# Performance work log

Measured on AMD Instinct MI355X. Metric: run time of the kernel, lower is better.

The kernel has to match this reference:

```python
import jax, jax.numpy as jnp
import numpy as np

B, L, D = 4, 4096, 256


def setup_inputs() -> dict:
    key = jax.random.key(0)
    kx, kq, kk, kv, ko = jax.random.split(key, 5)
    std = 0.02
    return {
        "x": jax.random.normal(kx, (B, L, D), dtype=jnp.float32),
        "Wq": std * jax.random.normal(kq, (D, D), dtype=jnp.float32),
        "Wk": std * jax.random.normal(kk, (D, D), dtype=jnp.float32),
        "Wv": std * jax.random.normal(kv, (D, D), dtype=jnp.float32),
        "Wo": std * jax.random.normal(ko, (D, D), dtype=jnp.float32),
    }


def reference(x, Wq, Wk, Wv, Wo):
    # nn.Linear(d,d,bias=False): y = x @ W.T
    q = x @ Wq.T  # [B,L,D]
    k = x @ Wk.T
    v = x @ Wv.T
    logits = jnp.einsum("bld,bmd->blm", q, k)  # [B,L,L], no 1/sqrt(d) scaling
    Lq = x.shape[1]
    causal_mask = jnp.triu(jnp.ones((Lq, Lq), dtype=bool), k=1)  # True above diag
    # ReLU attention: mask future to 0, relu, divide row i by max(i, 1)
    logits = jnp.where(causal_mask[None], jnp.asarray(0.0, logits.dtype), logits)
    attn = jax.nn.relu(logits)
    row_counts = jnp.maximum(jnp.arange(Lq, dtype=attn.dtype), 1.0)  # clamp_min(1)
    attn = attn / row_counts[None, :, None]
    ctx = jnp.einsum("blm,bmd->bld", attn, v)
    return ctx @ Wo.T
```

## Files before the change

kernel.cpp:

```cpp
#include <hip/hip_runtime.h>

#define BB 4
#define LL 4096
#define DD 256
#define MAXOFF 160

typedef short bf16x8 __attribute__((ext_vector_type(8)));
typedef short bf16x4 __attribute__((ext_vector_type(4)));
typedef float f32x4 __attribute__((ext_vector_type(4)));
typedef unsigned u32x4 __attribute__((ext_vector_type(4)));
typedef unsigned short u16;

__device__ inline u16 f2b(float f) {
    union { float f; unsigned u; } v; v.f = f;
    unsigned r = (v.u + 0x7fffu + ((v.u >> 16) & 1u)) >> 16;
    return (u16)r;
}
__device__ inline float b2f(short s) {
    union { unsigned u; float f; } v; v.u = ((unsigned)(unsigned short)s) << 16;
    return v.f;
}
__device__ inline unsigned pk2(float lo, float hi) {
    union { float f; unsigned u; } a, b; a.f = lo; b.f = hi;
    return __builtin_amdgcn_perm(b.u, a.u, 0x07060302u);
}

__device__ inline f32x4 mfma32(bf16x8 a, bf16x8 b, f32x4 c) {
    return __builtin_amdgcn_mfma_f32_16x16x32_bf16(a, b, c, 0, 0, 0);
}
__device__ inline f32x4 mfma16(bf16x4 a, bf16x4 b, f32x4 c) {
    return __builtin_amdgcn_mfma_f32_16x16x16bf16_1k(a, b, c, 0, 0, 0);
}

__device__ inline void gl_lds(const u16* g, u16* l) {
    __builtin_amdgcn_global_load_lds(
        (const __attribute__((address_space(1))) void*)g,
        (__attribute__((address_space(3))) void*)l, 16, 0, 0);
}


__global__ __launch_bounds__(256) void wconv_kernel(
    const float* __restrict__ Wq, const float* __restrict__ Wk,
    const float* __restrict__ Wv, const float* __restrict__ Wo,
    u16* __restrict__ wf, u16* __restrict__ wo16)
{
    const int w = threadIdx.x >> 6, lane = threadIdx.x & 63;
    const int q4 = lane >> 4, ln = lane & 15;
    const int id = blockIdx.x * 4 + w;
    const int mat = id >> 7, rem = id & 127, ct = rem >> 3, ks = rem & 7;
    if (mat < 3) {
        const float* W = (mat == 0) ? Wq : (mat == 1) ? Wk : Wv;
        const float* src = W + (size_t)(ct * 16 + ln) * DD + ks * 32 + q4 * 8;
        float4 f0 = ((const float4*)src)[0], f1 = ((const float4*)src)[1];
        bf16x8 t;
        t[0] = (short)f2b(f0.x); t[1] = (short)f2b(f0.y);
        t[2] = (short)f2b(f0.z); t[3] = (short)f2b(f0.w);
        t[4] = (short)f2b(f1.x); t[5] = (short)f2b(f1.y);
        t[6] = (short)f2b(f1.z); t[7] = (short)f2b(f1.w);
        *(bf16x8*)(wf + (size_t)mat * 65536 + (ct * 8 + ks) * 512 + lane * 8) = t;
    } else {
        const float* src = Wo + (size_t)(ct * 16 + ln) * DD + ks * 32 + q4 * 4;
        float4 f0 = *(const float4*)src;
        float4 f1 = *(const float4*)(src + 16);
        bf16x4 t0, t1;
        t0[0] = (short)f2b(f0.x); t0[1] = (short)f2b(f0.y);
        t0[2] = (short)f2b(f0.z); t0[3] = (short)f2b(f0.w);
        t1[0] = (short)f2b(f1.x); t1[1] = (short)f2b(f1.y);
        t1[2] = (short)f2b(f1.z); t1[3] = (short)f2b(f1.w);
        *(bf16x4*)(wo16 + (size_t)(ct * 16 + 2 * ks) * 256 + lane * 4) = t0;
        *(bf16x4*)(wo16 + (size_t)(ct * 16 + 2 * ks + 1) * 256 + lane * 4) = t1;
    }
}

__global__ __launch_bounds__(256, 4) void qkv_kernel(
    const float* __restrict__ x, const u16* __restrict__ wf,
    u16* __restrict__ qf, u16* __restrict__ kf_, u16* __restrict__ vf_)
{
    __shared__ u16 lt_q[32 * 136];
    __shared__ u16 lt_k[32 * 136];
    __shared__ u16 lt_v[128 * 40];

    const int w = threadIdx.x >> 6, lane = threadIdx.x & 63;
    const int q4 = lane >> 4, ln = lane & 15;
    const int tg = blockIdx.x >> 1, half = blockIdx.x & 1;
    const int tl = w & 1, dq = w >> 1;

    bf16x8 a[8];
    {
        const float* xrow = x + (size_t)(tg * 32 + tl * 16 + ln) * DD;
        #pragma unroll
        for (int ks = 0; ks < 8; ++ks) {
            const float4* p = (const float4*)(xrow + ks * 32 + q4 * 8);
            float4 f0 = p[0], f1 = p[1];
            bf16x8 t;
            t[0] = (short)f2b(f0.x); t[1] = (short)f2b(f0.y);
            t[2] = (short)f2b(f0.z); t[3] = (short)f2b(f0.w);
            t[4] = (short)f2b(f1.x); t[5] = (short)f2b(f1.y);
            t[6] = (short)f2b(f1.z); t[7] = (short)f2b(f1.w);
            a[ks] = t;
        }
    }

    f32x4 acc0[4], acc1[4], acc2[4];
    #pragma unroll
    for (int cl = 0; cl < 4; ++cl) {
        acc0[cl] = f32x4{0.f, 0.f, 0.f, 0.f};
        acc1[cl] = f32x4{0.f, 0.f, 0.f, 0.f};
        acc2[cl] = f32x4{0.f, 0.f, 0.f, 0.f};
    }

    #pragma unroll
    for (int ks = 0; ks < 8; ++ks) {
        #pragma unroll
        for (int cl = 0; cl < 4; ++cl) {
            const int ct = half * 8 + dq * 4 + cl;
            const size_t off = ((size_t)ct * 8 + ks) * 512 + lane * 8;
            bf16x8 b0 = *(const bf16x8*)(wf + off);
            bf16x8 b1 = *(const bf16x8*)(wf + 65536 + off);
            bf16x8 b2 = *(const bf16x8*)(wf + 131072 + off);
            acc0[cl] = mfma32(a[ks], b0, acc0[cl]);
            acc1[cl] = mfma32(a[ks], b1, acc1[cl]);
            acc2[cl] = mfma32(a[ks], b2, acc2[cl]);
        }
    }

    #pragma unroll
    for (int cl = 0; cl < 4; ++cl) {
        const int coll = (dq * 4 + cl) * 16 + ln;
        #pragma unroll
        for (int r = 0; r < 4; ++r) {
            const int tok = tl * 16 + q4 * 4 + r;
            lt_q[tok * 136 + coll] = f2b(acc0[cl][r]);
            lt_k[tok * 136 + coll] = f2b(acc1[cl][r]);
            lt_v[coll * 40 + tok] = f2b(acc2[cl][r]);
        }
    }
    __syncthreads();

    {
        const int h = w & 1;
        #pragma unroll
        for (int e = 0; e < 2; ++e) {
            const int ksl = 2 * dq + e;
            const int ks = half * 4 + ksl;
            bf16x8 aq = *(const bf16x8*)&lt_q[(h * 16 + ln) * 136 + ksl * 32 + q4 * 8];
            bf16x8 ak = *(const bf16x8*)&lt_k[(h * 16 + ln) * 136 + ksl * 32 + q4 * 8];
            const size_t dst = (size_t)((tg * 2 + h) * 8 + ks) * 512 + lane * 8;
            *(bf16x8*)(qf + dst) = aq;
            *(bf16x8*)(kf_ + dst) = ak;
        }
    }
    #pragma unroll
    for (int e = 0; e < 2; ++e) {
        const int dt_l = 2 * w + e;
        bf16x4 lo = *(const bf16x4*)&lt_v[(dt_l * 16 + ln) * 40 + q4 * 4];
        bf16x4 hi = *(const bf16x4*)&lt_v[(dt_l * 16 + ln) * 40 + 16 + q4 * 4];
        bf16x8 t;
        t[0] = lo[0]; t[1] = lo[1]; t[2] = lo[2]; t[3] = lo[3];
        t[4] = hi[0]; t[5] = hi[1]; t[6] = hi[2]; t[7] = hi[3];
        *(bf16x8*)(vf_ + (size_t)(tg * 16 + half * 8 + dt_l) * 512 + lane * 8) = t;
    }
}

__global__ __launch_bounds__(256, 2) void attn_kernel(
    const u16* __restrict__ qf, const u16* __restrict__ kfr,
    const u16* __restrict__ vfr, u16* __restrict__ part)
{
    __shared__ u16 buf[2][32][512];

    const int i = blockIdx.x;
    const int b = (i >> 1) & 3;
    const int j = ((i >> 3) << 1) | (i & 1);

    const int w = threadIdx.x >> 6, lane = threadIdx.x & 63;
    const int q4 = lane >> 4, ln = lane & 15;

    const int u0 = (33 * j) >> 1;
    const int u1 = (33 * (j + 1)) >> 1;

    int g = (int)((sqrtf((float)(2 * u0 + 1)) - 1.0f) * 0.5f);
    while (2 * (g + 1) * (g + 2) <= u0) ++g;
    while (2 * g * (g + 1) > u0) --g;
    int kt = u0 - 2 * g * (g + 1);
    int u = u0;

    int off = 0;
    for (int g2 = 0; g2 < g; ++g2) {
        const int j0 = (4 * g2 * (g2 + 1) + 1) / 33;
        const int jl = (4 * (g2 + 1) * (g2 + 2) - 1) / 33;
        off += jl - j0 + 1;
    }

    {
        const size_t cb = (size_t)((b * 128 + kt) * 16) * 512;
        #pragma unroll
        for (int c4 = 0; c4 < 8; ++c4) {
            const int c = w * 8 + c4;
            const u16* gsrc = ((c < 16) ? (kfr + cb + c * 512)
                                        : (vfr + cb + (c - 16) * 512)) + lane * 8;
            gl_lds(gsrc, &buf[u0 & 1][c][0]);
        }
    }

    while (u < u1) {
        const int ktend = 4 * g + 4;
        const int rem = u1 - u;
        const int kt_stop = (ktend < kt + rem) ? ktend : (kt + rem);
        const int t0 = g * 8 + 2 * w;
        const int qg0 = t0 * 16 + ln;
        const int qg1 = qg0 + 16;
        const float inv0 = 1.0f / (float)(qg0 > 1 ? qg0 : 1);
        const float inv1 = 1.0f / (float)qg1;

        bf16x8 qB0[8], qB1[8];
        {
            const u16* qb0 = qf + (size_t)(t0 * 8) * 512 + (size_t)b * (128 * 16 * 512) + lane * 8;
            #pragma unroll
            for (int ks = 0; ks < 8; ++ks) {
                qB0[ks] = *(const bf16x8*)(qb0 + ks * 512);
                qB1[ks] = *(const bf16x8*)(qb0 + (8 + ks) * 512);
            }
        }

        f32x4 oacc0[16], oacc1[16];
        #pragma unroll
        for (int dt = 0; dt < 16; ++dt) {
            oacc0[dt] = f32x4{0.f, 0.f, 0.f, 0.f};
            oacc1[dt] = f32x4{0.f, 0.f, 0.f, 0.f};
        }

        #pragma unroll 1
        for (; kt < kt_stop; ++kt, ++u) {
            const int cur = u & 1;
            __syncthreads();

            if (u + 1 < u1) {
                const int ktn = (kt + 1 < ktend) ? (kt + 1) : 0;
                const size_t cb = (size_t)((b * 128 + ktn) * 16) * 512;
                #pragma unroll
                for (int c4 = 0; c4 < 8; ++c4) {
                    const int c = w * 8 + c4;
                    const u16* gsrc = ((c < 16) ? (kfr + cb + c * 512)
                                                : (vfr + cb + (c - 16) * 512)) + lane * 8;
                    gl_lds(gsrc, &buf[cur ^ 1][c][0]);
                }
            }

            f32x4 s00 = f32x4{0.f, 0.f, 0.f, 0.f};
            f32x4 s10 = f32x4{0.f, 0.f, 0.f, 0.f};
            f32x4 s01 = f32x4{0.f, 0.f, 0.f, 0.f};
            f32x4 s11 = f32x4{0.f, 0.f, 0.f, 0.f};
            #pragma unroll
            for (int ks = 0; ks < 8; ++ks) {
                bf16x8 kf0 = *(const bf16x8*)&buf[cur][ks][lane * 8];
                bf16x8 kf1 = *(const bf16x8*)&buf[cur][8 + ks][lane * 8];
                s00 = mfma32(kf0, qB0[ks], s00);
                s10 = mfma32(kf1, qB0[ks], s10);
                s01 = mfma32(kf0, qB1[ks], s01);
                s11 = mfma32(kf1, qB1[ks], s11);
            }

            const int d0 = kt * 32 + q4 * 4 - qg0;
            float v00[4], v10[4], v01[4], v11[4];
            #pragma unroll
            for (int rr = 0; rr < 4; ++rr) {
                v00[rr] = (d0 + rr > 0)      ? 0.f : fmaxf(s00[rr], 0.f) * inv0;
                v10[rr] = (d0 + 16 + rr > 0) ? 0.f : fmaxf(s10[rr], 0.f) * inv0;
                v01[rr] = (d0 - 16 + rr > 0) ? 0.f : fmaxf(s01[rr], 0.f) * inv1;
                v11[rr] = (d0 + rr > 0)      ? 0.f : fmaxf(s11[rr], 0.f) * inv1;
            }
            union { u32x4 u; bf16x8 h; } c0, c1;
            c0.u[0] = pk2(v00[0], v00[1]); c0.u[1] = pk2(v00[2], v00[3]);
            c0.u[2] = pk2(v10[0], v10[1]); c0.u[3] = pk2(v10[2], v10[3]);
            c1.u[0] = pk2(v01[0], v01[1]); c1.u[1] = pk2(v01[2], v01[3]);
            c1.u[2] = pk2(v11[0], v11[1]); c1.u[3] = pk2(v11[2], v11[3]);

            #pragma unroll
            for (int dt = 0; dt < 16; ++dt) {
                bf16x8 vv = *(const bf16x8*)&buf[cur][16 + dt][lane * 8];
                oacc0[dt] = mfma32(vv, c0.h, oacc0[dt]);
                oacc1[dt] = mfma32(vv, c1.h, oacc1[dt]);
            }
        }

        {
            const int j0g = (4 * g * (g + 1) + 1) / 33;
            const int gslot = off + (j - j0g);
            u16* pb0 = part + ((((size_t)b * MAXOFF + gslot) * 8 + 2 * w) * 16) * 256 + lane * 4;
            u16* pb1 = pb0 + 16 * 256;
            #pragma unroll
            for (int dt = 0; dt < 16; ++dt) {
                bf16x4 t0v, t1v;
                t0v[0] = (short)f2b(oacc0[dt][0]); t0v[1] = (short)f2b(oacc0[dt][1]);
                t0v[2] = (short)f2b(oacc0[dt][2]); t0v[3] = (short)f2b(oacc0[dt][3]);
                t1v[0] = (short)f2b(oacc1[dt][0]); t1v[1] = (short)f2b(oacc1[dt][1]);
                t1v[2] = (short)f2b(oacc1[dt][2]); t1v[3] = (short)f2b(oacc1[dt][3]);
                *(bf16x4*)(pb0 + dt * 256) = t0v;
                *(bf16x4*)(pb1 + dt * 256) = t1v;
            }
            off += ((4 * (g + 1) * (g + 2) - 1) / 33) - j0g + 1;
        }
        ++g;
        kt = 0;
    }
}

__global__ __launch_bounds__(256, 4) void oproj_kernel(
    const u16* __restrict__ part, const u16* __restrict__ wo16,
    float* __restrict__ out)
{
    __shared__ u16 cb[16 * 256];

    const int w = threadIdx.x >> 6, lane = threadIdx.x & 63;
    const int q4 = lane >> 4, ln = lane & 15;
    const int g16 = blockIdx.x;
    const int b = g16 >> 8, gb = g16 & 255;
    const int g = gb >> 3;
    const int tloc = gb & 7;

    int off = 0;
    for (int g2 = 0; g2 < g; ++g2) {
        const int j0 = (4 * g2 * (g2 + 1) + 1) / 33;
        const int jl = (4 * (g2 + 1) * (g2 + 2) - 1) / 33;
        off += jl - j0 + 1;
    }
    const int j0g = (4 * g * (g + 1) + 1) / 33;
    const int jlg = (4 * (g + 1) * (g + 2) - 1) / 33;
    const int nsl = jlg - j0g + 1;

    #pragma unroll
    for (int c4 = 0; c4 < 4; ++c4) {
        const int dt = w * 4 + c4;
        f32x4 s = f32x4{0.f, 0.f, 0.f, 0.f};
        for (int sl = 0; sl < nsl; ++sl) {
            const u16* p = part + ((((size_t)b * MAXOFF + off + sl) * 8 + tloc) * 16 + dt) * 256 + lane * 4;
            bf16x4 pv = *(const bf16x4*)p;
            s[0] += b2f(pv[0]); s[1] += b2f(pv[1]);
            s[2] += b2f(pv[2]); s[3] += b2f(pv[3]);
        }
        bf16x4 t;
        t[0] = (short)f2b(s[0]); t[1] = (short)f2b(s[1]);
        t[2] = (short)f2b(s[2]); t[3] = (short)f2b(s[3]);
        *(bf16x4*)&cb[dt * 256 + lane * 4] = t;
    }
    __syncthreads();

    #pragma unroll
    for (int c4 = 0; c4 < 4; ++c4) {
        const int ct = w * 4 + c4;
        f32x4 acc = f32x4{0.f, 0.f, 0.f, 0.f};
        #pragma unroll
        for (int dt = 0; dt < 16; ++dt) {
            bf16x4 A = *(const bf16x4*)(wo16 + (size_t)(ct * 16 + dt) * 256 + lane * 4);
            bf16x4 B = *(const bf16x4*)&cb[dt * 256 + lane * 4];
            acc = mfma16(A, B, acc);
        }
        float* o = out + (size_t)(g16 * 16 + ln) * DD + ct * 16 + q4 * 4;
        *(f32x4*)o = acc;
    }
}

extern "C" void kernel_launch(void* const* d_in, const int* in_sizes, int n_in,
                              void* d_out, int out_size, void* d_ws, size_t ws_size,
                              hipStream_t stream)
{
    const float* x  = (const float*)d_in[0];
    const float* Wq = (const float*)d_in[1];
    const float* Wk = (const float*)d_in[2];
    const float* Wv = (const float*)d_in[3];
    const float* Wo = (const float*)d_in[4];
    float* out = (float*)d_out;

    const size_t nW = (size_t)DD * DD;
    const size_t nX = (size_t)BB * LL * DD;

    u16* wf   = (u16*)d_ws;
    u16* wo16 = wf + 3 * nW;
    u16* qfr  = wf + 4 * nW;
    u16* kfr  = qfr + nX;
    u16* vfr  = kfr + nX;
    u16* part = vfr + nX;

    wconv_kernel<<<dim3(128), dim3(256), 0, stream>>>(Wq, Wk, Wv, Wo, wf, wo16);
    qkv_kernel<<<dim3(1024), dim3(256), 0, stream>>>(x, wf, qfr, kfr, vfr);
    attn_kernel<<<dim3(512), dim3(256), 0, stream>>>(qfr, kfr, vfr, part);
    oproj_kernel<<<dim3(1024), dim3(256), 0, stream>>>(part, wo16, out);
}
```

Baseline: 158.5 us.

## Software-pipeline attention loop: overlap previous PV with current QK and split K/V buffers

```diff
diff --git a/kernel.cpp b/kernel.cpp
--- a/kernel.cpp
+++ b/kernel.cpp
@@ -166,7 +166,8 @@
     const u16* __restrict__ qf, const u16* __restrict__ kfr,
     const u16* __restrict__ vfr, u16* __restrict__ part)
 {
-    __shared__ u16 buf[2][32][512];
+    __shared__ u16 kbuf[2][16][512];
+    __shared__ u16 vbuf[2][16][512];
 
     const int i = blockIdx.x;
     const int b = (i >> 1) & 3;
@@ -182,7 +183,6 @@
     while (2 * (g + 1) * (g + 2) <= u0) ++g;
     while (2 * g * (g + 1) > u0) --g;
     int kt = u0 - 2 * g * (g + 1);
-    int u = u0;
 
     int off = 0;
     for (int g2 = 0; g2 < g; ++g2) {
@@ -194,72 +194,119 @@
     {
         const size_t cb = (size_t)((b * 128 + kt) * 16) * 512;
         #pragma unroll
-        for (int c4 = 0; c4 < 8; ++c4) {
-            const int c = w * 8 + c4;
-            const u16* gsrc = ((c < 16) ? (kfr + cb + c * 512)
-                                        : (vfr + cb + (c - 16) * 512)) + lane * 8;
-            gl_lds(gsrc, &buf[u0 & 1][c][0]);
-        }
-    }
-
-    while (u < u1) {
-        const int ktend = 4 * g + 4;
-        const int rem = u1 - u;
-        const int kt_stop = (ktend < kt + rem) ? ktend : (kt + rem);
+        for (int c4 = 0; c4 < 4; ++c4) {
+            const int c = w * 4 + c4;
+            gl_lds(kfr + cb + c * 512 + lane * 8, &kbuf[u0 & 1][c][0]);
+        }
+    }
+
+    int qg0;
+    float inv0, inv1;
+    bf16x8 qB0[8], qB1[8];
+    f32x4 oacc0[16], oacc1[16];
+    union { u32x4 u; bf16x8 h; } c0, c1;
+
+    auto load_group = [&]() {
         const int t0 = g * 8 + 2 * w;
-        const int qg0 = t0 * 16 + ln;
-        const int qg1 = qg0 + 16;
-        const float inv0 = 1.0f / (float)(qg0 > 1 ? qg0 : 1);
-        const float inv1 = 1.0f / (float)qg1;
-
-        bf16x8 qB0[8], qB1[8];
-        {
-            const u16* qb0 = qf + (size_t)(t0 * 8) * 512 + (size_t)b * (128 * 16 * 512) + lane * 8;
-            #pragma unroll
-            for (int ks = 0; ks < 8; ++ks) {
-                qB0[ks] = *(const bf16x8*)(qb0 + ks * 512);
-                qB1[ks] = *(const bf16x8*)(qb0 + (8 + ks) * 512);
-            }
-        }
-
-        f32x4 oacc0[16], oacc1[16];
+        qg0 = t0 * 16 + ln;
+        inv0 = 1.0f / (float)(qg0 > 1 ? qg0 : 1);
+        inv1 = 1.0f / (float)(qg0 + 16);
+        const u16* qb0 = qf + (size_t)(t0 * 8) * 512 + (size_t)b * (128 * 16 * 512) + lane * 8;
+        #pragma unroll
+        for (int ks = 0; ks < 8; ++ks) {
+            qB0[ks] = *(const bf16x8*)(qb0 + ks * 512);
+            qB1[ks] = *(const bf16x8*)(qb0 + (8 + ks) * 512);
+        }
         #pragma unroll
         for (int dt = 0; dt < 16; ++dt) {
             oacc0[dt] = f32x4{0.f, 0.f, 0.f, 0.f};
             oacc1[dt] = f32x4{0.f, 0.f, 0.f, 0.f};
         }
-
-        #pragma unroll 1
-        for (; kt < kt_stop; ++kt, ++u) {
-            const int cur = u & 1;
-            __syncthreads();
-
-            if (u + 1 < u1) {
-                const int ktn = (kt + 1 < ktend) ? (kt + 1) : 0;
-                const size_t cb = (size_t)((b * 128 + ktn) * 16) * 512;
-                #pragma unroll
-                for (int c4 = 0; c4 < 8; ++c4) {
-                    const int c = w * 8 + c4;
-                    const u16* gsrc = ((c < 16) ? (kfr + cb + c * 512)
-                                                : (vfr + cb + (c - 16) * 512)) + lane * 8;
-                    gl_lds(gsrc, &buf[cur ^ 1][c][0]);
-                }
+    };
+
+    auto do_pv = [&](int pb) {
+        #pragma unroll
+        for (int dt = 0; dt < 16; ++dt) {
+            bf16x8 vv = *(const bf16x8*)&vbuf[pb][dt][lane * 8];
+            oacc0[dt] = mfma32(vv, c0.h, oacc0[dt]);
+            oacc1[dt] = mfma32(vv, c1.h, oacc1[dt]);
+        }
+    };
+
+    auto do_epilogue = [&](int fg) {
+        const int j0g = (4 * fg * (fg + 1) + 1) / 33;
+        const int gslot = off + (j - j0g);
+        u16* pb0 = part + ((((size_t)b * MAXOFF + gslot) * 8 + 2 * w) * 16) * 256 + lane * 4;
+        u16* pb1 = pb0 + 16 * 256;
+        #pragma unroll
+        for (int dt = 0; dt < 16; ++dt) {
+            bf16x4 t0v, t1v;
+            t0v[0] = (short)f2b(oacc0[dt][0]); t0v[1] = (short)f2b(oacc0[dt][1]);
+            t0v[2] = (short)f2b(oacc0[dt][2]); t0v[3] = (short)f2b(oacc0[dt][3]);
+            t1v[0] = (short)f2b(oacc1[dt][0]); t1v[1] = (short)f2b(oacc1[dt][1]);
+            t1v[2] = (short)f2b(oacc1[dt][2]); t1v[3] = (short)f2b(oacc1[dt][3]);
+            *(bf16x4*)(pb0 + dt * 256) = t0v;
+            *(bf16x4*)(pb1 + dt * 256) = t1v;
+        }
+        off += ((4 * (fg + 1) * (fg + 2) - 1) / 33) - j0g + 1;
+    };
+
+    load_group();
+    int flush_g = g;
+    bool havePrev = false;
+    bool flushPend = false;
+
+    #pragma unroll 1
+    for (int u = u0; u < u1; ++u) {
+        __syncthreads();
+
+        {
+            const size_t cbV = (size_t)((b * 128 + kt) * 16) * 512;
+            #pragma unroll
+            for (int c4 = 0; c4 < 4; ++c4) {
+                const int c = w * 4 + c4;
+                gl_lds(vfr + cbV + c * 512 + lane * 8, &vbuf[u & 1][c][0]);
             }
-
-            f32x4 s00 = f32x4{0.f, 0.f, 0.f, 0.f};
-            f32x4 s10 = f32x4{0.f, 0.f, 0.f, 0.f};
-            f32x4 s01 = f32x4{0.f, 0.f, 0.f, 0.f};
-            f32x4 s11 = f32x4{0.f, 0.f, 0.f, 0.f};
+        }
+        if (u + 1 < u1) {
+            const int ktn = (kt + 1 < 4 * g + 4) ? (kt + 1) : 0;
+            const size_t cbK = (size_t)((b * 128 + ktn) * 16) * 512;
             #pragma unroll
-            for (int ks = 0; ks < 8; ++ks) {
-                bf16x8 kf0 = *(const bf16x8*)&buf[cur][ks][lane * 8];
-                bf16x8 kf1 = *(const bf16x8*)&buf[cur][8 + ks][lane * 8];
-                s00 = mfma32(kf0, qB0[ks], s00);
-                s10 = mfma32(kf1, qB0[ks], s10);
-                s01 = mfma32(kf0, qB1[ks], s01);
-                s11 = mfma32(kf1, qB1[ks], s11);
+            for (int c4 = 0; c4 < 4; ++c4) {
+                const int c = w * 4 + c4;
+                gl_lds(kfr + cbK + c * 512 + lane * 8, &kbuf[(u + 1) & 1][c][0]);
             }
-
+        }
+
+        if (flushPend) {
+            __builtin_amdgcn_s_setprio(1);
+            do_pv((u - 1) & 1);
+            __builtin_amdgcn_s_setprio(0);
+            do_epilogue(flush_g);
+            load_group();
+            flush_g = g;
+            havePrev = false;
+            flushPend = false;
+        }
+
+        f32x4 s00 = f32x4{0.f, 0.f, 0.f, 0.f};
+        f32x4 s10 = f32x4{0.f, 0.f, 0.f, 0.f};
+        f32x4 s01 = f32x4{0.f, 0.f, 0.f, 0.f};
+        f32x4 s11 = f32x4{0.f, 0.f, 0.f, 0.f};
+        __builtin_amdgcn_s_setprio(1);
+        #pragma unroll
+        for (int ks = 0; ks < 8; ++ks) {
+            bf16x8 kf0 = *(const bf16x8*)&kbuf[u & 1][ks][lane * 8];
+            bf16x8 kf1 = *(const bf16x8*)&kbuf[u & 1][8 + ks][lane * 8];
+            s00 = mfma32(kf0, qB0[ks], s00);
+            s10 = mfma32(kf1, qB0[ks], s10);
+            s01 = mfma32(kf0, qB1[ks], s01);
+            s11 = mfma32(kf1, qB1[ks], s11);
+        }
+        if (havePrev) do_pv((u - 1) & 1);
+        __builtin_amdgcn_s_setprio(0);
+
+        {
             const int d0 = kt * 32 + q4 * 4 - qg0;
             float v00[4], v10[4], v01[4], v11[4];
             #pragma unroll
@@ -269,40 +316,22 @@
                 v01[rr] = (d0 - 16 + rr > 0) ? 0.f : fmaxf(s01[rr], 0.f) * inv1;
                 v11[rr] = (d0 + rr > 0)      ? 0.f : fmaxf(s11[rr], 0.f) * inv1;
             }
-            union { u32x4 u; bf16x8 h; } c0, c1;
             c0.u[0] = pk2(v00[0], v00[1]); c0.u[1] = pk2(v00[2], v00[3]);
             c0.u[2] = pk2(v10[0], v10[1]); c0.u[3] = pk2(v10[2], v10[3]);
             c1.u[0] = pk2(v01[0], v01[1]); c1.u[1] = pk2(v01[2], v01[3]);
             c1.u[2] = pk2(v11[0], v11[1]); c1.u[3] = pk2(v11[2], v11[3]);
-
-            #pragma unroll
-            for (int dt = 0; dt < 16; ++dt) {
-                bf16x8 vv = *(const bf16x8*)&buf[cur][16 + dt][lane * 8];
-                oacc0[dt] = mfma32(vv, c0.h, oacc0[dt]);
-                oacc1[dt] = mfma32(vv, c1.h, oacc1[dt]);
-            }
-        }
-
-        {
-            const int j0g = (4 * g * (g + 1) + 1) / 33;
-            const int gslot = off + (j - j0g);
-            u16* pb0 = part + ((((size_t)b * MAXOFF + gslot) * 8 + 2 * w) * 16) * 256 + lane * 4;
-            u16* pb1 = pb0 + 16 * 256;
-            #pragma unroll
-            for (int dt = 0; dt < 16; ++dt) {
-                bf16x4 t0v, t1v;
-                t0v[0] = (short)f2b(oacc0[dt][0]); t0v[1] = (short)f2b(oacc0[dt][1]);
-                t0v[2] = (short)f2b(oacc0[dt][2]); t0v[3] = (short)f2b(oacc0[dt][3]);
-                t1v[0] = (short)f2b(oacc1[dt][0]); t1v[1] = (short)f2b(oacc1[dt][1]);
-                t1v[2] = (short)f2b(oacc1[dt][2]); t1v[3] = (short)f2b(oacc1[dt][3]);
-                *(bf16x4*)(pb0 + dt * 256) = t0v;
-                *(bf16x4*)(pb1 + dt * 256) = t1v;
-            }
-            off += ((4 * (g + 1) * (g + 2) - 1) / 33) - j0g + 1;
-        }
-        ++g;
-        kt = 0;
-    }
+        }
+        havePrev = true;
+
+        ++kt;
+        if (kt == 4 * g + 4) { kt = 0; ++g; flushPend = true; }
+    }
+
+    __syncthreads();
+    __builtin_amdgcn_s_setprio(1);
+    do_pv((u1 - 1) & 1);
+    __builtin_amdgcn_s_setprio(0);
+    do_epilogue(flush_g);
 }
 
 __global__ __launch_bounds__(256, 4) void oproj_kernel(
```

Result: slower. 167.7 us (+5.8%).
